# Optimization experiments

Hardware: AMD Instinct MI355X
Metric: run time of the kernel (lower is better)

Reference implementation:

```python
import jax, jax.numpy as jnp
import numpy as np

NBITS = 3      # weight LSQ bits
PBITS = 8      # partial-sum LSQ bits
EPS = 1e-5


def round_ste(x):
    # straight-through round: identity gradient
    return x + jax.lax.stop_gradient(jnp.round(x) - x)


def lsq(x, alpha, nbits):
    # learned-step-size quantize/dequantize (symmetric signed)
    qn = -(2 ** (nbits - 1))
    qp = 2 ** (nbits - 1) - 1
    return round_ste(jnp.clip(x / alpha, qn, qp)) * alpha


def split_views(x):
    # x: [B,C,H,W] -> 9 shifted views of the 1-padded input, stacked [9,B,C,H,W]
    B, C, H, W = x.shape
    xp = jnp.pad(x, ((0, 0), (0, 0), (1, 1), (1, 1)))
    views = [xp[:, :, di:di + H, dj:dj + W] for dj in range(3) for di in range(3)]
    return jnp.stack(views, 0)


def split_conv3x3(x, w, wa, pa):
    # 3x3 conv emulated as 9 shifted 1x1 LSQ convs with quantized partial-sum accumulate
    # w: [9,O,C] per-tap 1x1 weights, wa: [9] weight step sizes, pa: [9] psum step sizes
    xs = split_views(x)                                      # [9,B,C,H,W]
    wq = jax.vmap(lambda wk, ak: lsq(wk, ak, NBITS))(w, wa)  # [9,O,C]
    ps = jnp.einsum('kbchw,koc->kbohw', xs, wq)              # 9 partial sums
    psq = lsq(ps, pa[:, None, None, None, None], PBITS)      # PartialSumLSQ each tap
    return psq.sum(0)                                        # accumulate -> [B,O,H,W]


def batchnorm(x, g, b):
    m = x.mean((0, 2, 3), keepdims=True)
    v = x.var((0, 2, 3), keepdims=True)
    return (x - m) / jnp.sqrt(v + EPS) * g[None, :, None, None] + b[None, :, None, None]


def setup_inputs() -> dict:
    key = jax.random.key(0)
    ks = jax.random.split(key, 8)
    B, C, O, H, W = 16, 128, 128, 56, 56
    x = jax.random.normal(ks[0], (B, C, H, W), jnp.float32)
    w1 = jax.random.normal(ks[1], (9, O, C), jnp.float32) * 0.05
    w2 = jax.random.normal(ks[2], (9, O, O), jnp.float32) * 0.05
    qp_w = 2 ** (NBITS - 1) - 1
    wa1 = 2.0 * jnp.mean(jnp.abs(w1), axis=(1, 2)) / np.sqrt(qp_w)
    wa2 = 2.0 * jnp.mean(jnp.abs(w2), axis=(1, 2)) / np.sqrt(qp_w)
    pa1 = jnp.full((9,), 0.05, jnp.float32)
    pa2 = jnp.full((9,), 0.05, jnp.float32)
    g1 = jnp.ones((O,), jnp.float32); b1 = jnp.zeros((O,), jnp.float32)
    g2 = jnp.ones((O,), jnp.float32); b2 = jnp.zeros((O,), jnp.float32)
    return {'x': x, 'w1': w1, 'wa1': wa1, 'pa1': pa1, 'g1': g1, 'b1': b1,
            'w2': w2, 'wa2': wa2, 'pa2': pa2, 'g2': g2, 'b2': b2}


def reference(x, w1, wa1, pa1, g1, b1, w2, wa2, pa2, g2, b2):
    identity = x
    out = split_conv3x3(x, w1, wa1, pa1)
    out = jax.nn.relu(batchnorm(out, g1, b1))
    out = split_conv3x3(out, w2, wa2, pa2)
    out = batchnorm(out, g2, b2)
    return jax.nn.relu(out + identity)
```

## Files before the change

kernel.cpp:

```cpp
#include <hip/hip_runtime.h>
#include <math.h>

typedef _Float16 f16;
typedef _Float16 half8 __attribute__((ext_vector_type(8)));
typedef float floatx4 __attribute__((ext_vector_type(4)));
typedef unsigned int u32;

#define B_   16
#define C_   128
#define O_   128
#define H_   56
#define W_   56
#define HW_  3136
#define NPIX 50176
#define NPC  50176.0f
#define NELEM 6422528
#define NW_  147456

typedef __attribute__((address_space(3))) u32 lds_u32;
typedef __attribute__((address_space(1))) u32 glb_u32;
__device__ __forceinline__ void async_copy16(const void* g, void* l) {
    __builtin_amdgcn_global_load_lds((const glb_u32*)g, (lds_u32*)l, 16, 0, 0);
}

__global__ __launch_bounds__(256) void prep_kernel(
        const float* __restrict__ w1, const float* __restrict__ wa1,
        const float* __restrict__ w2, const float* __restrict__ wa2,
        f16* __restrict__ q1, f16* __restrict__ q2) {
    int idx = blockIdx.x * 256 + threadIdx.x;
    if (idx < NW_) {
        float a = wa1[idx >> 14];
        q1[idx] = (f16)rintf(fminf(fmaxf(w1[idx] / a, -4.f), 3.f));
    } else {
        int j = idx - NW_;
        float a = wa2[j >> 14];
        q2[j] = (f16)rintf(fminf(fmaxf(w2[j] / a, -4.f), 3.f));
    }
}

__global__ __launch_bounds__(256) void transpose_split_kernel(
        const float* __restrict__ x, f16* __restrict__ xh, f16* __restrict__ xl,
        float* __restrict__ aux) {
    __shared__ f16 hs[64][136];
    __shared__ f16 ls[64][136];
    const int t = threadIdx.x;
    const int blk = blockIdx.x;
    if (blk == 0) { for (int i = t; i < 1152; i += 256) aux[i] = 0.f; }
    const int b = blk / 49;
    const int p0 = (blk - b * 49) * 64;
    #pragma unroll
    for (int i = 0; i < 8; ++i) {
        const int c = i * 16 + (t >> 4);
        const int px = (t & 15) * 4;
        const float4 v = *(const float4*)&x[((size_t)(b * C_ + c)) * HW_ + p0 + px];
        const float vv[4] = {v.x, v.y, v.z, v.w};
        #pragma unroll
        for (int j = 0; j < 4; ++j) {
            f16 h = (f16)vv[j];
            hs[px + j][c] = h;
            ls[px + j][c] = (f16)(vv[j] - (float)h);
        }
    }
    __syncthreads();
    const int px = t >> 2, seg = t & 3;
    const size_t ob = ((size_t)(b * HW_ + p0 + px)) * 128 + seg * 32;
    #pragma unroll
    for (int k = 0; k < 4; ++k) {
        *(half8*)(xh + ob + k * 8) = *(const half8*)&hs[px][seg * 32 + k * 8];
        *(half8*)(xl + ob + k * 8) = *(const half8*)&ls[px][seg * 32 + k * 8];
    }
}

__global__ __launch_bounds__(256, 2) void conv_mfma_kernel(
        const f16* __restrict__ xh, const f16* __restrict__ xl,
        const f16* __restrict__ wq, const float* __restrict__ wav,
        const float* __restrict__ pav, const f16* __restrict__ zp,
        float* __restrict__ cout, float* __restrict__ stats) {
    __shared__ f16 As[2][128][64];
    __shared__ f16 Bs[128][128];
    const int t = threadIdx.x;
    const int lane = t & 63;
    const int wv = t >> 6;
    const int wm = wv & 1, wn = wv >> 1;
    const int tile = blockIdx.x;

    int abase_[4], ah_[4], aw_[4], gbyteA[4];
    #pragma unroll
    for (int i = 0; i < 4; ++i) {
        const int r = wv * 32 + i * 8 + (lane >> 3);
        const int gp = tile * 128 + r;
        const int b = gp / HW_;
        const int p = gp - b * HW_;
        const int h = p / W_;
        const int w = p - h * W_;
        abase_[i] = b * HW_; ah_[i] = h; aw_[i] = w;
        gbyteA[i] = (((lane & 7) ^ (r & 7)) << 4);
    }
    int boff[8];
    #pragma unroll
    for (int i = 0; i < 8; ++i) {
        const int r = wv * 32 + i * 4 + (lane >> 4);
        const int g = (lane & 15) ^ (r & 15);
        boff[i] = r * 256 + g * 16;
    }
    const int ardbase = (wm * 64 + (lane & 15)) * 128;
    const char* Bbase = (const char*)&Bs[0][0] + (wn * 64 + (lane & 15)) * 256;
    int acol[2], bcol[2][2];
    #pragma unroll
    for (int ks = 0; ks < 2; ++ks) {
        acol[ks] = (((ks * 4 + (lane >> 4)) ^ (lane & 7)) << 4);
        bcol[0][ks] = (((ks * 4 + (lane >> 4)) ^ (lane & 15)) << 4);
        bcol[1][ks] = (((8 + ks * 4 + (lane >> 4)) ^ (lane & 15)) << 4);
    }

    floatx4 acc[4][4];
    floatx4 facc[4][4];
    const floatx4 z4 = {0.f, 0.f, 0.f, 0.f};
    #pragma unroll
    for (int mt = 0; mt < 4; ++mt)
        #pragma unroll
        for (int nt = 0; nt < 4; ++nt) facc[mt][nt] = z4;

    int aoff[4];
    const char* zpc = (const char*)zp;

    auto stageA = [&](int j, int bf) {
        const char* plane = (const char*)((j & 1) ? xl : xh);
        const int khb = (j >> 1) << 7;
        #pragma unroll
        for (int i = 0; i < 4; ++i) {
            const char* g = (aoff[i] >= 0) ? plane + aoff[i] + khb + gbyteA[i]
                                           : zpc + gbyteA[i];
            async_copy16(g, (void*)&As[bf][wv * 32 + i * 8][0]);
        }
    };

    for (int tap = 0; tap < 9; ++tap) {
        const int di = tap - (tap / 3) * 3 - 1;
        const int dj = tap / 3 - 1;
        const float pak = pav[tap];
        const float s1 = wav[tap] / pak;

        #pragma unroll
        for (int i = 0; i < 4; ++i) {
            const int hp = ah_[i] + di, wp = aw_[i] + dj;
            const bool v = ((unsigned)hp < (unsigned)H_) && ((unsigned)wp < (unsigned)W_);
            aoff[i] = v ? ((abase_[i] + hp * W_ + wp) << 8) : -1;
        }
        #pragma unroll
        for (int mt = 0; mt < 4; ++mt)
            #pragma unroll
            for (int nt = 0; nt < 4; ++nt) acc[mt][nt] = z4;

        const char* wt = (const char*)wq + (tap << 15);
        #pragma unroll
        for (int i = 0; i < 8; ++i)
            async_copy16(wt + boff[i], (void*)&Bs[wv * 32 + i * 4][0]);
        stageA(0, 0);
        __syncthreads();

        for (int j = 0; j < 4; ++j) {
            if (j < 3) stageA(j + 1, (j + 1) & 1);
            const char* Ab = (const char*)&As[j & 1][0][0] + ardbase;
            const int kh = j >> 1;
            #pragma unroll
            for (int ks = 0; ks < 2; ++ks) {
                half8 af[4], bf4[4];
                #pragma unroll
                for (int mt = 0; mt < 4; ++mt)
                    af[mt] = *(const half8*)(Ab + mt * 2048 + acol[ks]);
                #pragma unroll
                for (int nt = 0; nt < 4; ++nt)
                    bf4[nt] = *(const half8*)(Bbase + nt * 4096 + bcol[kh][ks]);
                #pragma unroll
                for (int nt = 0; nt < 4; ++nt)
                    #pragma unroll
                    for (int mt = 0; mt < 4; ++mt)
                        acc[mt][nt] = __builtin_amdgcn_mfma_f32_16x16x32_f16(
                            af[mt], bf4[nt], acc[mt][nt], 0, 0, 0);
            }
            __syncthreads();
        }

        #pragma unroll
        for (int mt = 0; mt < 4; ++mt)
            #pragma unroll
            for (int nt = 0; nt < 4; ++nt) {
                #pragma unroll
                for (int e = 0; e < 4; ++e) {
                    float q = rintf(fminf(fmaxf(acc[mt][nt][e] * s1, -128.f), 127.f));
                    facc[mt][nt][e] = fmaf(q, pak, facc[mt][nt][e]);
                }
            }
    }

    const int gp0 = tile * 128 + wm * 64;
    const int ocb = wn * 64 + (lane & 15);
    #pragma unroll
    for (int mt = 0; mt < 4; ++mt)
        #pragma unroll
        for (int e = 0; e < 4; ++e) {
            const int gp = gp0 + mt * 16 + ((lane >> 4) << 2) + e;
            float* rp = cout + (size_t)gp * 128 + ocb;
            rp[0]  = facc[mt][0][e];
            rp[16] = facc[mt][1][e];
            rp[32] = facc[mt][2][e];
            rp[48] = facc[mt][3][e];
        }

    float* red = (float*)&As[0][0][0];
    float sv[4], qv[4];
    #pragma unroll
    for (int nt = 0; nt < 4; ++nt) {
        float s = 0.f, q = 0.f;
        #pragma unroll
        for (int mt = 0; mt < 4; ++mt)
            #pragma unroll
            for (int e = 0; e < 4; ++e) {
                const float v = facc[mt][nt][e];
                s += v; q = fmaf(v, v, q);
            }
        s += __shfl_xor(s, 16, 64); s += __shfl_xor(s, 32, 64);
        q += __shfl_xor(q, 16, 64); q += __shfl_xor(q, 32, 64);
        sv[nt] = s; qv[nt] = q;
    }
    if (lane < 16) {
        #pragma unroll
        for (int nt = 0; nt < 4; ++nt) {
            const int oc = wn * 64 + nt * 16 + lane;
            red[oc * 2 + wm] = sv[nt];
            red[512 + oc * 2 + wm] = qv[nt];
        }
    }
    __syncthreads();
    if (t < 128) {
        atomicAdd(&stats[t],       red[2 * t] + red[2 * t + 1]);
        atomicAdd(&stats[128 + t], red[512 + 2 * t] + red[512 + 2 * t + 1]);
    }
}

__global__ void bnprep_kernel(const float* __restrict__ stats,
        const float* __restrict__ g, const float* __restrict__ bb,
        float* __restrict__ coef) {
    const int t = threadIdx.x;
    const float m = stats[t] * (1.f / NPC);
    const float var = stats[128 + t] * (1.f / NPC) - m * m;
    const float inv = 1.f / sqrtf(var + 1e-5f);
    const float sc = g[t] * inv;
    coef[t] = sc;
    coef[128 + t] = bb[t] - m * sc;
}

__global__ __launch_bounds__(256) void bn_split_kernel(
        const float* __restrict__ cin, const float* __restrict__ coef,
        f16* __restrict__ xh, f16* __restrict__ xl) {
    const int idx = blockIdx.x * 256 + threadIdx.x;
    const size_t base = (size_t)idx * 8;
    const int oc0 = (idx & 15) * 8;
    const float4 va = *(const float4*)(cin + base);
    const float4 vb = *(const float4*)(cin + base + 4);
    const float4 s0 = *(const float4*)(coef + oc0);
    const float4 s1 = *(const float4*)(coef + oc0 + 4);
    const float4 h0 = *(const float4*)(coef + 128 + oc0);
    const float4 h1 = *(const float4*)(coef + 128 + oc0 + 4);
    float y[8];
    y[0] = fmaxf(fmaf(va.x, s0.x, h0.x), 0.f);
    y[1] = fmaxf(fmaf(va.y, s0.y, h0.y), 0.f);
    y[2] = fmaxf(fmaf(va.z, s0.z, h0.z), 0.f);
    y[3] = fmaxf(fmaf(va.w, s0.w, h0.w), 0.f);
    y[4] = fmaxf(fmaf(vb.x, s1.x, h1.x), 0.f);
    y[5] = fmaxf(fmaf(vb.y, s1.y, h1.y), 0.f);
    y[6] = fmaxf(fmaf(vb.z, s1.z, h1.z), 0.f);
    y[7] = fmaxf(fmaf(vb.w, s1.w, h1.w), 0.f);
    half8 hv, lv;
    #pragma unroll
    for (int j = 0; j < 8; ++j) {
        f16 hh = (f16)y[j];
        hv[j] = hh;
        lv[j] = (f16)(y[j] - (float)hh);
    }
    *(half8*)(xh + base) = hv;
    *(half8*)(xl + base) = lv;
}

__global__ __launch_bounds__(256) void final_kernel(
        const float* __restrict__ cin, const float* __restrict__ coef,
        const float* __restrict__ resid, float* __restrict__ out) {
    __shared__ float ts[128][68];
    const int t = threadIdx.x;
    const int blk = blockIdx.x;
    const int b = blk / 49;
    const int p0 = (blk - b * 49) * 64;
    #pragma unroll
    for (int i = 0; i < 8; ++i) {
        const int lin = i * 256 + t;
        const int px = lin >> 5;
        const int oc = (lin & 31) * 4;
        const float4 v = *(const float4*)&cin[((size_t)(b * HW_ + p0 + px)) * 128 + oc];
        const float4 sc = *(const float4*)&coef[oc];
        const float4 sh = *(const float4*)&coef[128 + oc];
        ts[oc + 0][px] = fmaf(v.x, sc.x, sh.x);
        ts[oc + 1][px] = fmaf(v.y, sc.y, sh.y);
        ts[oc + 2][px] = fmaf(v.z, sc.z, sh.z);
        ts[oc + 3][px] = fmaf(v.w, sc.w, sh.w);
    }
    __syncthreads();
    #pragma unroll
    for (int i = 0; i < 2; ++i) {
        const int c = i * 64 + (t >> 2);
        const int px = (t & 3) * 16;
        const size_t go = ((size_t)(b * C_ + c)) * HW_ + p0 + px;
        #pragma unroll
        for (int k = 0; k < 4; ++k) {
            float4 v = *(const float4*)&ts[c][px + k * 4];
            const float4 r = *(const float4*)&resid[go + k * 4];
            v.x = fmaxf(v.x + r.x, 0.f);
            v.y = fmaxf(v.y + r.y, 0.f);
            v.z = fmaxf(v.z + r.z, 0.f);
            v.w = fmaxf(v.w + r.w, 0.f);
            *(float4*)&out[go + k * 4] = v;
        }
    }
}

extern "C" void kernel_launch(void* const* d_in, const int* in_sizes, int n_in,
                              void* d_out, int out_size, void* d_ws, size_t ws_size,
                              hipStream_t stream) {
    const float* x   = (const float*)d_in[0];
    const float* w1  = (const float*)d_in[1];
    const float* wa1 = (const float*)d_in[2];
    const float* pa1 = (const float*)d_in[3];
    const float* g1  = (const float*)d_in[4];
    const float* b1  = (const float*)d_in[5];
    const float* w2  = (const float*)d_in[6];
    const float* wa2 = (const float*)d_in[7];
    const float* pa2 = (const float*)d_in[8];
    const float* g2  = (const float*)d_in[9];
    const float* b2  = (const float*)d_in[10];
    float* out = (float*)d_out;

    char* ws = (char*)d_ws;
    f16* xh  = (f16*)ws;
    f16* xl  = (f16*)(ws + 12845056);
    f16* wq1 = (f16*)(ws + 25690112);
    f16* wq2 = (f16*)(ws + 25690112 + 294912);
    float* cbuf = (float*)(ws + 25690112 + 2 * 294912);
    float* aux  = (float*)(ws + 25690112 + 2 * 294912 + 25690112);
    float* stats1 = aux;
    float* stats2 = aux + 256;
    float* coef1  = aux + 512;
    float* coef2  = aux + 768;
    const f16* zp = (const f16*)(aux + 1024);

    hipLaunchKernelGGL(prep_kernel, dim3(1152), dim3(256), 0, stream,
                       w1, wa1, w2, wa2, wq1, wq2);
    hipLaunchKernelGGL(transpose_split_kernel, dim3(784), dim3(256), 0, stream,
                       x, xh, xl, aux);
    hipLaunchKernelGGL(conv_mfma_kernel, dim3(392), dim3(256), 0, stream,
                       xh, xl, wq1, wa1, pa1, zp, cbuf, stats1);
    hipLaunchKernelGGL(bnprep_kernel, dim3(1), dim3(128), 0, stream,
                       stats1, g1, b1, coef1);
    hipLaunchKernelGGL(bn_split_kernel, dim3(3136), dim3(256), 0, stream,
                       cbuf, coef1, xh, xl);
    hipLaunchKernelGGL(conv_mfma_kernel, dim3(392), dim3(256), 0, stream,
                       xh, xl, wq2, wa2, pa2, zp, cbuf, stats2);
    hipLaunchKernelGGL(bnprep_kernel, dim3(1), dim3(128), 0, stream,
                       stats2, g2, b2, coef2);
    hipLaunchKernelGGL(final_kernel, dim3(784), dim3(256), 0, stream,
                       cbuf, coef2, x, out);
}
```

Measured before the change: 228.3 us.

## Halve conv M-tile to 64 pixels and fold BN coefficient prep into consumers

The conv MFMA kernel now processes 64-pixel tiles instead of 128, doubling the grid to 784 blocks and raising the launch-bounds occupancy hint to 3 blocks per CU. This gives better load balance across CUs and lower register and LDS use per block, at the cost of restaging the full weight tile for half as much compute. Separately, the single-block bnprep kernels are removed: each bn_split and final block now computes the BN scale and shift from the stats into shared memory, cutting two tiny launches at the price of redundant per-block work.

```diff
diff --git a/kernel.cpp b/kernel.cpp
--- a/kernel.cpp
+++ b/kernel.cpp
@@ -45,7 +45,7 @@
     __shared__ f16 ls[64][136];
     const int t = threadIdx.x;
     const int blk = blockIdx.x;
-    if (blk == 0) { for (int i = t; i < 1152; i += 256) aux[i] = 0.f; }
+    if (blk == 0) { for (int i = t; i < 640; i += 256) aux[i] = 0.f; }
     const int b = blk / 49;
     const int p0 = (blk - b * 49) * 64;
     #pragma unroll
@@ -71,12 +71,12 @@
     }
 }
 
-__global__ __launch_bounds__(256, 2) void conv_mfma_kernel(
+__global__ __launch_bounds__(256, 3) void conv_mfma_kernel(
         const f16* __restrict__ xh, const f16* __restrict__ xl,
         const f16* __restrict__ wq, const float* __restrict__ wav,
         const float* __restrict__ pav, const f16* __restrict__ zp,
         float* __restrict__ cout, float* __restrict__ stats) {
-    __shared__ f16 As[2][128][64];
+    __shared__ f16 As[2][64][64];
     __shared__ f16 Bs[128][128];
     const int t = threadIdx.x;
     const int lane = t & 63;
@@ -84,11 +84,11 @@
     const int wm = wv & 1, wn = wv >> 1;
     const int tile = blockIdx.x;
 
-    int abase_[4], ah_[4], aw_[4], gbyteA[4];
-    #pragma unroll
-    for (int i = 0; i < 4; ++i) {
-        const int r = wv * 32 + i * 8 + (lane >> 3);
-        const int gp = tile * 128 + r;
+    int abase_[2], ah_[2], aw_[2], gbyteA[2];
+    #pragma unroll
+    for (int i = 0; i < 2; ++i) {
+        const int r = i * 32 + wv * 8 + (lane >> 3);
+        const int gp = tile * 64 + r;
         const int b = gp / HW_;
         const int p = gp - b * HW_;
         const int h = p / W_;
@@ -103,7 +103,7 @@
         const int g = (lane & 15) ^ (r & 15);
         boff[i] = r * 256 + g * 16;
     }
-    const int ardbase = (wm * 64 + (lane & 15)) * 128;
+    const int ardbase = (wm * 32 + (lane & 15)) * 128;
     const char* Bbase = (const char*)&Bs[0][0] + (wn * 64 + (lane & 15)) * 256;
     int acol[2], bcol[2][2];
     #pragma unroll
@@ -113,25 +113,25 @@
         bcol[1][ks] = (((8 + ks * 4 + (lane >> 4)) ^ (lane & 15)) << 4);
     }
 
-    floatx4 acc[4][4];
-    floatx4 facc[4][4];
+    floatx4 acc[2][4];
+    floatx4 facc[2][4];
     const floatx4 z4 = {0.f, 0.f, 0.f, 0.f};
     #pragma unroll
-    for (int mt = 0; mt < 4; ++mt)
+    for (int mt = 0; mt < 2; ++mt)
         #pragma unroll
         for (int nt = 0; nt < 4; ++nt) facc[mt][nt] = z4;
 
-    int aoff[4];
+    int aoff[2];
     const char* zpc = (const char*)zp;
 
     auto stageA = [&](int j, int bf) {
         const char* plane = (const char*)((j & 1) ? xl : xh);
         const int khb = (j >> 1) << 7;
         #pragma unroll
-        for (int i = 0; i < 4; ++i) {
+        for (int i = 0; i < 2; ++i) {
             const char* g = (aoff[i] >= 0) ? plane + aoff[i] + khb + gbyteA[i]
                                            : zpc + gbyteA[i];
-            async_copy16(g, (void*)&As[bf][wv * 32 + i * 8][0]);
+            async_copy16(g, (void*)&As[bf][i * 32 + wv * 8][0]);
         }
     };
 
@@ -142,13 +142,13 @@
         const float s1 = wav[tap] / pak;
 
         #pragma unroll
-        for (int i = 0; i < 4; ++i) {
+        for (int i = 0; i < 2; ++i) {
             const int hp = ah_[i] + di, wp = aw_[i] + dj;
             const bool v = ((unsigned)hp < (unsigned)H_) && ((unsigned)wp < (unsigned)W_);
             aoff[i] = v ? ((abase_[i] + hp * W_ + wp) << 8) : -1;
         }
         #pragma unroll
-        for (int mt = 0; mt < 4; ++mt)
+        for (int mt = 0; mt < 2; ++mt)
             #pragma unroll
             for (int nt = 0; nt < 4; ++nt) acc[mt][nt] = z4;
 
@@ -165,9 +165,9 @@
             const int kh = j >> 1;
             #pragma unroll
             for (int ks = 0; ks < 2; ++ks) {
-                half8 af[4], bf4[4];
+                half8 af[2], bf4[4];
                 #pragma unroll
-                for (int mt = 0; mt < 4; ++mt)
+                for (int mt = 0; mt < 2; ++mt)
                     af[mt] = *(const half8*)(Ab + mt * 2048 + acol[ks]);
                 #pragma unroll
                 for (int nt = 0; nt < 4; ++nt)
@@ -175,7 +175,7 @@
                 #pragma unroll
                 for (int nt = 0; nt < 4; ++nt)
                     #pragma unroll
-                    for (int mt = 0; mt < 4; ++mt)
+                    for (int mt = 0; mt < 2; ++mt)
                         acc[mt][nt] = __builtin_amdgcn_mfma_f32_16x16x32_f16(
                             af[mt], bf4[nt], acc[mt][nt], 0, 0, 0);
             }
@@ -183,7 +183,7 @@
         }
 
         #pragma unroll
-        for (int mt = 0; mt < 4; ++mt)
+        for (int mt = 0; mt < 2; ++mt)
             #pragma unroll
             for (int nt = 0; nt < 4; ++nt) {
                 #pragma unroll
@@ -194,10 +194,10 @@
             }
     }
 
-    const int gp0 = tile * 128 + wm * 64;
+    const int gp0 = tile * 64 + wm * 32;
     const int ocb = wn * 64 + (lane & 15);
     #pragma unroll
-    for (int mt = 0; mt < 4; ++mt)
+    for (int mt = 0; mt < 2; ++mt)
         #pragma unroll
         for (int e = 0; e < 4; ++e) {
             const int gp = gp0 + mt * 16 + ((lane >> 4) << 2) + e;
@@ -214,7 +214,7 @@
     for (int nt = 0; nt < 4; ++nt) {
         float s = 0.f, q = 0.f;
         #pragma unroll
-        for (int mt = 0; mt < 4; ++mt)
+        for (int mt = 0; mt < 2; ++mt)
             #pragma unroll
             for (int e = 0; e < 4; ++e) {
                 const float v = facc[mt][nt][e];
@@ -239,30 +239,30 @@
     }
 }
 
-__global__ void bnprep_kernel(const float* __restrict__ stats,
+__global__ __launch_bounds__(256) void bn_split_kernel(
+        const float* __restrict__ cin, const float* __restrict__ stats,
         const float* __restrict__ g, const float* __restrict__ bb,
-        float* __restrict__ coef) {
+        f16* __restrict__ xh, f16* __restrict__ xl) {
+    __shared__ float sc_s[128], sh_s[128];
     const int t = threadIdx.x;
-    const float m = stats[t] * (1.f / NPC);
-    const float var = stats[128 + t] * (1.f / NPC) - m * m;
-    const float inv = 1.f / sqrtf(var + 1e-5f);
-    const float sc = g[t] * inv;
-    coef[t] = sc;
-    coef[128 + t] = bb[t] - m * sc;
-}
-
-__global__ __launch_bounds__(256) void bn_split_kernel(
-        const float* __restrict__ cin, const float* __restrict__ coef,
-        f16* __restrict__ xh, f16* __restrict__ xl) {
-    const int idx = blockIdx.x * 256 + threadIdx.x;
+    if (t < 128) {
+        const float m = stats[t] * (1.f / NPC);
+        const float var = stats[128 + t] * (1.f / NPC) - m * m;
+        const float inv = 1.f / sqrtf(var + 1e-5f);
+        const float sc = g[t] * inv;
+        sc_s[t] = sc;
+        sh_s[t] = bb[t] - m * sc;
+    }
+    __syncthreads();
+    const int idx = blockIdx.x * 256 + t;
     const size_t base = (size_t)idx * 8;
     const int oc0 = (idx & 15) * 8;
     const float4 va = *(const float4*)(cin + base);
     const float4 vb = *(const float4*)(cin + base + 4);
-    const float4 s0 = *(const float4*)(coef + oc0);
-    const float4 s1 = *(const float4*)(coef + oc0 + 4);
-    const float4 h0 = *(const float4*)(coef + 128 + oc0);
-    const float4 h1 = *(const float4*)(coef + 128 + oc0 + 4);
+    const float4 s0 = *(const float4*)(sc_s + oc0);
+    const float4 s1 = *(const float4*)(sc_s + oc0 + 4);
+    const float4 h0 = *(const float4*)(sh_s + oc0);
+    const float4 h1 = *(const float4*)(sh_s + oc0 + 4);
     float y[8];
     y[0] = fmaxf(fmaf(va.x, s0.x, h0.x), 0.f);
     y[1] = fmaxf(fmaf(va.y, s0.y, h0.y), 0.f);
@@ -284,10 +284,21 @@
 }
 
 __global__ __launch_bounds__(256) void final_kernel(
-        const float* __restrict__ cin, const float* __restrict__ coef,
+        const float* __restrict__ cin, const float* __restrict__ stats,
+        const float* __restrict__ g, const float* __restrict__ bb,
         const float* __restrict__ resid, float* __restrict__ out) {
     __shared__ float ts[128][68];
+    __shared__ float sc_s[128], sh_s[128];
     const int t = threadIdx.x;
+    if (t < 128) {
+        const float m = stats[t] * (1.f / NPC);
+        const float var = stats[128 + t] * (1.f / NPC) - m * m;
+        const float inv = 1.f / sqrtf(var + 1e-5f);
+        const float sc = g[t] * inv;
+        sc_s[t] = sc;
+        sh_s[t] = bb[t] - m * sc;
+    }
+    __syncthreads();
     const int blk = blockIdx.x;
     const int b = blk / 49;
     const int p0 = (blk - b * 49) * 64;
@@ -297,8 +308,8 @@
         const int px = lin >> 5;
         const int oc = (lin & 31) * 4;
         const float4 v = *(const float4*)&cin[((size_t)(b * HW_ + p0 + px)) * 128 + oc];
-        const float4 sc = *(const float4*)&coef[oc];
-        const float4 sh = *(const float4*)&coef[128 + oc];
+        const float4 sc = *(const float4*)&sc_s[oc];
+        const float4 sh = *(const float4*)&sh_s[oc];
         ts[oc + 0][px] = fmaf(v.x, sc.x, sh.x);
         ts[oc + 1][px] = fmaf(v.y, sc.y, sh.y);
         ts[oc + 2][px] = fmaf(v.z, sc.z, sh.z);
@@ -348,24 +359,18 @@
     float* aux  = (float*)(ws + 25690112 + 2 * 294912 + 25690112);
     float* stats1 = aux;
     float* stats2 = aux + 256;
-    float* coef1  = aux + 512;
-    float* coef2  = aux + 768;
-    const f16* zp = (const f16*)(aux + 1024);
+    const f16* zp = (const f16*)(aux + 512);
 
     hipLaunchKernelGGL(prep_kernel, dim3(1152), dim3(256), 0, stream,
                        w1, wa1, w2, wa2, wq1, wq2);
     hipLaunchKernelGGL(transpose_split_kernel, dim3(784), dim3(256), 0, stream,
                        x, xh, xl, aux);
-    hipLaunchKernelGGL(conv_mfma_kernel, dim3(392), dim3(256), 0, stream,
+    hipLaunchKernelGGL(conv_mfma_kernel, dim3(784), dim3(256), 0, stream,
                        xh, xl, wq1, wa1, pa1, zp, cbuf, stats1);
-    hipLaunchKernelGGL(bnprep_kernel, dim3(1), dim3(128), 0, stream,
-                       stats1, g1, b1, coef1);
     hipLaunchKernelGGL(bn_split_kernel, dim3(3136), dim3(256), 0, stream,
-                       cbuf, coef1, xh, xl);
-    hipLaunchKernelGGL(conv_mfma_kernel, dim3(392), dim3(256), 0, stream,
+                       cbuf, stats1, g1, b1, xh, xl);
+    hipLaunchKernelGGL(conv_mfma_kernel, dim3(784), dim3(256), 0, stream,
                        xh, xl, wq2, wa2, pa2, zp, cbuf, stats2);
-    hipLaunchKernelGGL(bnprep_kernel, dim3(1), dim3(128), 0, stream,
-                       stats2, g2, b2, coef2);
     hipLaunchKernelGGL(final_kernel, dim3(784), dim3(256), 0, stream,
-                       cbuf, coef2, x, out);
-}
+                       cbuf, stats2, g2, b2, x, out);
+}
```

Result: slower. 281.4 us (+23.3%).
